# Kernel optimization log

Measured on AMD Instinct MI355X. Metric: run time of the kernel, lower is better.

## Reference

```python
import jax, jax.numpy as jnp
import numpy as np

N = 100000   # num_embeddings
D = 128      # embedding_dims
E = 128      # edge_output_size
S = 2048     # number of streaming interactions
W_DECAY = 1.0  # Decayer w, decay_method='exp': f(dt) = exp(-w*dt)


def setup_inputs() -> dict:
    key = jax.random.key(0)
    ks = jax.random.split(key, 20)
    def nrm(k, shape, s):
        return jax.random.normal(k, shape, jnp.float32) * s
    sD = 1.0 / np.sqrt(D)
    sE = 1.0 / np.sqrt(E)
    return {
        'heads': jax.random.randint(ks[0], (S,), 0, N, dtype=jnp.int32),
        'tails': jax.random.randint(ks[1], (S,), 0, N, dtype=jnp.int32),
        'times': jnp.sort(jax.random.uniform(ks[2], (S,), jnp.float32) * 100.0),
        # node state tables (nn.Embedding weights in the original)
        'node_rep': nrm(ks[3], (N, D), 0.1),
        'cell_head': nrm(ks[4], (N, D), 0.1),
        'hidden_head': nrm(ks[5], (N, D), 0.1),
        'cell_tail': nrm(ks[6], (N, D), 0.1),
        'hidden_tail': nrm(ks[7], (N, D), 0.1),
        # Edge_updater_nn head / tail: act(rep_h @ W1 + rep_t @ W2 + b)
        'Weh1': nrm(ks[8], (D, E), sD), 'Weh2': nrm(ks[9], (D, E), sD), 'beh': jnp.zeros((E,), jnp.float32),
        'Wet1': nrm(ks[10], (D, E), sD), 'Wet2': nrm(ks[11], (D, E), sD), 'bet': jnp.zeros((E,), jnp.float32),
        # TLSTM head (time-decayed LSTM cell)
        'Wxh': nrm(ks[12], (E, 4 * D), sE), 'Whh': nrm(ks[13], (D, 4 * D), sD), 'bh': jnp.zeros((4 * D,), jnp.float32),
        'Wdh': nrm(ks[14], (D, D), sD), 'bdh': jnp.zeros((D,), jnp.float32),
        # TLSTM tail
        'Wxt': nrm(ks[15], (E, 4 * D), sE), 'Wht': nrm(ks[16], (D, 4 * D), sD), 'bt': jnp.zeros((4 * D,), jnp.float32),
        'Wdt': nrm(ks[17], (D, D), sD), 'bdt': jnp.zeros((D,), jnp.float32),
        # Combiner: tanh(h_head @ Wc1 + h_tail @ Wc2)
        'Wc1': nrm(ks[18], (D, D), sD), 'Wc2': nrm(ks[19], (D, D), sD),
    }


def _tlstm(x, c, h, decay, Wx, Wh, b, Wd, bd):
    # Time-aware LSTM: decompose short-term memory, decay it by elapsed time, recombine.
    cs = jnp.tanh(c @ Wd + bd)      # short-term memory component
    c_adj = c - cs + cs * decay      # adjusted previous cell
    z = x @ Wx + h @ Wh + b          # [4D] gate pre-activations
    i, f, o, g = jnp.split(z, 4)
    i = jax.nn.sigmoid(i); f = jax.nn.sigmoid(f); o = jax.nn.sigmoid(o)
    g = jnp.tanh(g)
    c_new = f * c_adj + i * g
    h_new = o * jnp.tanh(c_new)
    return c_new, h_new


def reference(heads, tails, times, node_rep, cell_head, hidden_head, cell_tail, hidden_tail,
              Weh1, Weh2, beh, Wet1, Wet2, bet,
              Wxh, Whh, bh, Wdh, bdh, Wxt, Wht, bt, Wdt, bdt, Wc1, Wc2):
    recent = jnp.zeros((node_rep.shape[0],), jnp.float32)  # recent_timestamp, init 0

    def step(state, ev):
        rep, ch, hh, ct, ht, rt = state
        h_i, t_i, tm = ev
        rep_h = rep[h_i]                    # gather current reps
        rep_t = rep[t_i]
        dec_h = jnp.exp(-W_DECAY * (tm - rt[h_i]))   # decayer(delta_t)
        dec_t = jnp.exp(-W_DECAY * (tm - rt[t_i]))
        edge_h = jnp.tanh(rep_h @ Weh1 + rep_t @ Weh2 + beh)  # edge_updater_head
        edge_t = jnp.tanh(rep_h @ Wet1 + rep_t @ Wet2 + bet)  # edge_updater_tail
        c_h, h_h = _tlstm(edge_h, ch[h_i], hh[h_i], dec_h, Wxh, Whh, bh, Wdh, bdh)
        c_t, h_t = _tlstm(edge_t, ct[t_i], ht[t_i], dec_t, Wxt, Wht, bt, Wdt, bdt)
        new_rep_h = jnp.tanh(h_h @ Wc1 + ht[h_i] @ Wc2)  # combiner(head hidden, tail hidden)
        new_rep_t = jnp.tanh(hh[t_i] @ Wc1 + h_t @ Wc2)
        # scatter updated state (head written before tail, matching original ordering)
        rep = rep.at[h_i].set(new_rep_h).at[t_i].set(new_rep_t)
        ch = ch.at[h_i].set(c_h); hh = hh.at[h_i].set(h_h)
        ct = ct.at[t_i].set(c_t); ht = ht.at[t_i].set(h_t)
        rt = rt.at[h_i].set(tm).at[t_i].set(tm)
        # if_updated=0: emit pre-update representations for this interaction
        return (rep, ch, hh, ct, ht, rt), (rep_h, rep_t)

    state0 = (node_rep, cell_head, hidden_head, cell_tail, hidden_tail, recent)
    _, (out_h, out_t) = jax.lax.scan(step, state0, (heads, tails, times))
    return jnp.stack([out_h, out_t])  # [2, S, D]
```

## Files before the change

kernel.cpp:

```cpp
#include <hip/hip_runtime.h>
#include <hip/hip_cooperative_groups.h>
#include <math.h>

namespace cg = cooperative_groups;

#define DD 128
#define G 8
#define TPB 512
#define NBLK_MAX 256
#define SMAX 2048

__device__ __forceinline__ float sigmoidf(float x) { return 1.0f / (1.0f + expf(-x)); }

__global__ __launch_bounds__(64) void pred_kernel(
    const int* __restrict__ heads, const int* __restrict__ tails, int S,
    int* __restrict__ ph, int* __restrict__ pt) {
  const int j = blockIdx.x;
  if (j >= S) return;
  const int myh = heads[j], myt = tails[j];
  const int lane = threadIdx.x;
  int mph = -1, mpt = -1;
#pragma unroll 4
  for (int i = lane; i < j; i += 64) {
    int a = heads[i], b = tails[i];
    if (a == myh || b == myh) mph = i;
    if (a == myt || b == myt) mpt = i;
  }
#pragma unroll
  for (int off = 32; off > 0; off >>= 1) {
    mph = max(mph, __shfl_down(mph, off));
    mpt = max(mpt, __shfl_down(mpt, off));
  }
  if (lane == 0) { ph[j] = mph; pt[j] = mpt; }
}

__global__ __launch_bounds__(1024) void finalize_kernel(
    int S, const int* __restrict__ phg, const int* __restrict__ ptg,
    int* __restrict__ order, int* __restrict__ level_off, int* __restrict__ n_levels) {
  __shared__ int lvl[SMAX], ph[SMAX], pt[SMAX], cnt[SMAX];
  __shared__ int changed, maxl;
  const int tid = threadIdx.x;

  for (int j = tid; j < S; j += 1024) { ph[j] = phg[j]; pt[j] = ptg[j]; lvl[j] = 1; }
  __syncthreads();

  for (int it = 0; it < S + 2; ++it) {
    if (tid == 0) changed = 0;
    __syncthreads();
    for (int j = tid; j < S; j += 1024) {
      int l = 1;
      int a = ph[j]; if (a >= 0) l = lvl[a] + 1;
      int b = pt[j]; if (b >= 0) { int lb = lvl[b] + 1; if (lb > l) l = lb; }
      if (l != lvl[j]) { lvl[j] = l; changed = 1; }
    }
    __syncthreads();
    if (!changed) break;
    __syncthreads();
  }

  if (tid == 0) maxl = 0;
  __syncthreads();
  for (int j = tid; j < S; j += 1024) atomicMax(&maxl, lvl[j]);
  __syncthreads();
  const int M = maxl;

  for (int l = tid; l < M; l += 1024) cnt[l] = 0;
  __syncthreads();
  for (int j = tid; j < S; j += 1024) atomicAdd(&cnt[lvl[j] - 1], 1);
  __syncthreads();
  if (tid == 0) {
    int run = 0;
    level_off[0] = 0;
    for (int l = 0; l < M; ++l) { run += cnt[l]; level_off[l + 1] = run; }
    n_levels[0] = M;
  }
  __syncthreads();

  for (int l = tid; l < M; l += 1024) cnt[l] = 0;
  __syncthreads();
  for (int j = tid; j < S; j += 1024) {
    int lv = lvl[j] - 1;
    int pos = level_off[lv] + atomicAdd(&cnt[lv], 1);
    order[pos] = j;
  }
}

struct PParams {
  const int* heads; const int* tails; const float* times;
  float* node_rep; float* cell_head; float* hidden_head; float* cell_tail; float* hidden_tail;
  const float* Weh1; const float* Weh2; const float* beh;
  const float* Wet1; const float* Wet2; const float* bet;
  const float* Wxh; const float* Whh; const float* bh; const float* Wdh; const float* bdh;
  const float* Wxt; const float* Wht; const float* bt; const float* Wdt; const float* bdt;
  const float* Wc1; const float* Wc2;
  float* out; float* rt;
  const int* order; const int* level_off; const int* n_levels;
  int S;
};

__global__ __launch_bounds__(TPB) void process_kernel(PParams p) {
  cg::grid_group grid = cg::this_grid();
  const int tid = threadIdx.x;
  const int d0 = (int)((blockIdx.x * 37u) & 127u);

  __shared__ __align__(16) float S_[16384];
  __shared__ int sIdx[G], hIdx[G], tIdx[G];
  __shared__ float tmv[G], decHs[G], decTs[G];

  const int O_REPH = 0,    O_REPT = 1024, O_CHS = 2048, O_CTS = 3072;
  const int O_ZH   = 0,    O_ZT   = 4096;
  const int O_HHS  = 8192, O_HTS  = 9216, O_HTH = 10240, O_HHT = 11264;
  const int O_EH   = 12288, O_ET  = 13312;
  const int O_CAH  = 14336, O_CAT = 15360;

  int nlv = p.n_levels[0];
  if (nlv < 0) nlv = 0;
  if (nlv > SMAX) nlv = SMAX;

  for (int lv = 0; lv < nlv; ++lv) {
    const int beg = p.level_off[lv], end = p.level_off[lv + 1];

    for (int base = beg + (int)blockIdx.x * G; base < end; base += (int)gridDim.x * G) {
      const int ng = min(G, end - base);
      __syncthreads();
      if (tid < ng) {
        int s = p.order[base + tid]; sIdx[tid] = s;
        int h = p.heads[s], t = p.tails[s];
        hIdx[tid] = h; tIdx[tid] = t;
        float tm = p.times[s]; tmv[tid] = tm;
        decHs[tid] = expf(-(tm - p.rt[h]));
        decTs[tid] = expf(-(tm - p.rt[t]));
      }
      __syncthreads();

      {
        const int d = tid & 127;
        for (int g = tid >> 7; g < ng; g += 4) {
          const size_t oh = (size_t)hIdx[g] * DD + d;
          const size_t ot = (size_t)tIdx[g] * DD + d;
          const int b = d * 8 + g;
          float rh = p.node_rep[oh];
          S_[O_REPH + b] = rh; p.out[(size_t)sIdx[g] * DD + d] = rh;
          S_[O_CHS + b] = p.cell_head[oh];
          S_[O_HHS + b] = p.hidden_head[oh];
          S_[O_HTH + b] = p.hidden_tail[oh];
          float rt_ = p.node_rep[ot];
          S_[O_REPT + b] = rt_; p.out[(size_t)(p.S + sIdx[g]) * DD + d] = rt_;
          S_[O_CTS + b] = p.cell_tail[ot];
          S_[O_HTS + b] = p.hidden_tail[ot];
          S_[O_HHT + b] = p.hidden_head[ot];
        }
      }
      __syncthreads();

      {
        const int role = tid >> 7, e = tid & 127;
        if (role == 0) {
          float bv = p.beh[e];
          float a[8];
#pragma unroll
          for (int g = 0; g < 8; ++g) a[g] = bv;
#pragma unroll 8
          for (int i = 0; i < DD; ++i) {
            const int d = (i + d0) & 127;
            float w1 = p.Weh1[d * DD + e], w2 = p.Weh2[d * DD + e];
            float4 rh0 = *(const float4*)&S_[O_REPH + d * 8];
            float4 rh1 = *(const float4*)&S_[O_REPH + d * 8 + 4];
            float4 rt0 = *(const float4*)&S_[O_REPT + d * 8];
            float4 rt1 = *(const float4*)&S_[O_REPT + d * 8 + 4];
            a[0] += rh0.x * w1 + rt0.x * w2; a[1] += rh0.y * w1 + rt0.y * w2;
            a[2] += rh0.z * w1 + rt0.z * w2; a[3] += rh0.w * w1 + rt0.w * w2;
            a[4] += rh1.x * w1 + rt1.x * w2; a[5] += rh1.y * w1 + rt1.y * w2;
            a[6] += rh1.z * w1 + rt1.z * w2; a[7] += rh1.w * w1 + rt1.w * w2;
          }
          float4 o0, o1;
          o0.x = tanhf(a[0]); o0.y = tanhf(a[1]); o0.z = tanhf(a[2]); o0.w = tanhf(a[3]);
          o1.x = tanhf(a[4]); o1.y = tanhf(a[5]); o1.z = tanhf(a[6]); o1.w = tanhf(a[7]);
          *(float4*)&S_[O_EH + e * 8] = o0;
          *(float4*)&S_[O_EH + e * 8 + 4] = o1;
        } else if (role == 1) {
          float bv = p.bet[e];
          float a[8];
#pragma unroll
          for (int g = 0; g < 8; ++g) a[g] = bv;
#pragma unroll 8
          for (int i = 0; i < DD; ++i) {
            const int d = (i + d0) & 127;
            float w1 = p.Wet1[d * DD + e], w2 = p.Wet2[d * DD + e];
            float4 rh0 = *(const float4*)&S_[O_REPH + d * 8];
            float4 rh1 = *(const float4*)&S_[O_REPH + d * 8 + 4];
            float4 rt0 = *(const float4*)&S_[O_REPT + d * 8];
            float4 rt1 = *(const float4*)&S_[O_REPT + d * 8 + 4];
            a[0] += rh0.x * w1 + rt0.x * w2; a[1] += rh0.y * w1 + rt0.y * w2;
            a[2] += rh0.z * w1 + rt0.z * w2; a[3] += rh0.w * w1 + rt0.w * w2;
            a[4] += rh1.x * w1 + rt1.x * w2; a[5] += rh1.y * w1 + rt1.y * w2;
            a[6] += rh1.z * w1 + rt1.z * w2; a[7] += rh1.w * w1 + rt1.w * w2;
          }
          float4 o0, o1;
          o0.x = tanhf(a[0]); o0.y = tanhf(a[1]); o0.z = tanhf(a[2]); o0.w = tanhf(a[3]);
          o1.x = tanhf(a[4]); o1.y = tanhf(a[5]); o1.z = tanhf(a[6]); o1.w = tanhf(a[7]);
          *(float4*)&S_[O_ET + e * 8] = o0;
          *(float4*)&S_[O_ET + e * 8 + 4] = o1;
        } else if (role == 2) {
          float bv = p.bdh[e];
          float a[8];
#pragma unroll
          for (int g = 0; g < 8; ++g) a[g] = bv;
#pragma unroll 8
          for (int i = 0; i < DD; ++i) {
            const int d = (i + d0) & 127;
            float wd = p.Wdh[d * DD + e];
            float4 c0 = *(const float4*)&S_[O_CHS + d * 8];
            float4 c1 = *(const float4*)&S_[O_CHS + d * 8 + 4];
            a[0] += c0.x * wd; a[1] += c0.y * wd; a[2] += c0.z * wd; a[3] += c0.w * wd;
            a[4] += c1.x * wd; a[5] += c1.y * wd; a[6] += c1.z * wd; a[7] += c1.w * wd;
          }
          float o[8];
#pragma unroll
          for (int g = 0; g < 8; ++g) {
            float cs = tanhf(a[g]);
            o[g] = S_[O_CHS + e * 8 + g] - cs + cs * decHs[g];
          }
          *(float4*)&S_[O_CAH + e * 8]     = make_float4(o[0], o[1], o[2], o[3]);
          *(float4*)&S_[O_CAH + e * 8 + 4] = make_float4(o[4], o[5], o[6], o[7]);
        } else {
          float bv = p.bdt[e];
          float a[8];
#pragma unroll
          for (int g = 0; g < 8; ++g) a[g] = bv;
#pragma unroll 8
          for (int i = 0; i < DD; ++i) {
            const int d = (i + d0) & 127;
            float wd = p.Wdt[d * DD + e];
            float4 c0 = *(const float4*)&S_[O_CTS + d * 8];
            float4 c1 = *(const float4*)&S_[O_CTS + d * 8 + 4];
            a[0] += c0.x * wd; a[1] += c0.y * wd; a[2] += c0.z * wd; a[3] += c0.w * wd;
            a[4] += c1.x * wd; a[5] += c1.y * wd; a[6] += c1.z * wd; a[7] += c1.w * wd;
          }
          float o[8];
#pragma unroll
          for (int g = 0; g < 8; ++g) {
            float cs = tanhf(a[g]);
            o[g] = S_[O_CTS + e * 8 + g] - cs + cs * decTs[g];
          }
          *(float4*)&S_[O_CAT + e * 8]     = make_float4(o[0], o[1], o[2], o[3]);
          *(float4*)&S_[O_CAT + e * 8 + 4] = make_float4(o[4], o[5], o[6], o[7]);
        }
      }
      __syncthreads();

      {
        const int c = tid;
        float bhv = p.bh[c], btv = p.bt[c];
        float h[8], t8[8];
#pragma unroll
        for (int g = 0; g < 8; ++g) { h[g] = bhv; t8[g] = btv; }
#pragma unroll 4
        for (int i = 0; i < DD; ++i) {
          const int d = (i + d0) & 127;
          float wxh = p.Wxh[d * 512 + c], whh = p.Whh[d * 512 + c];
          float wxt = p.Wxt[d * 512 + c], wht = p.Wht[d * 512 + c];
          float4 ex0 = *(const float4*)&S_[O_EH + d * 8];
          float4 ex1 = *(const float4*)&S_[O_EH + d * 8 + 4];
          float4 hx0 = *(const float4*)&S_[O_HHS + d * 8];
          float4 hx1 = *(const float4*)&S_[O_HHS + d * 8 + 4];
          float4 et0 = *(const float4*)&S_[O_ET + d * 8];
          float4 et1 = *(const float4*)&S_[O_ET + d * 8 + 4];
          float4 ht0 = *(const float4*)&S_[O_HTS + d * 8];
          float4 ht1 = *(const float4*)&S_[O_HTS + d * 8 + 4];
          h[0] += ex0.x * wxh + hx0.x * whh; h[1] += ex0.y * wxh + hx0.y * whh;
          h[2] += ex0.z * wxh + hx0.z * whh; h[3] += ex0.w * wxh + hx0.w * whh;
          h[4] += ex1.x * wxh + hx1.x * whh; h[5] += ex1.y * wxh + hx1.y * whh;
          h[6] += ex1.z * wxh + hx1.z * whh; h[7] += ex1.w * wxh + hx1.w * whh;
          t8[0] += et0.x * wxt + ht0.x * wht; t8[1] += et0.y * wxt + ht0.y * wht;
          t8[2] += et0.z * wxt + ht0.z * wht; t8[3] += et0.w * wxt + ht0.w * wht;
          t8[4] += et1.x * wxt + ht1.x * wht; t8[5] += et1.y * wxt + ht1.y * wht;
          t8[6] += et1.z * wxt + ht1.z * wht; t8[7] += et1.w * wxt + ht1.w * wht;
        }
        *(float4*)&S_[O_ZH + c * 8]     = make_float4(h[0], h[1], h[2], h[3]);
        *(float4*)&S_[O_ZH + c * 8 + 4] = make_float4(h[4], h[5], h[6], h[7]);
        *(float4*)&S_[O_ZT + c * 8]     = make_float4(t8[0], t8[1], t8[2], t8[3]);
        *(float4*)&S_[O_ZT + c * 8 + 4] = make_float4(t8[4], t8[5], t8[6], t8[7]);
      }
      __syncthreads();

      {
        const int side = tid >> 8, sub = (tid >> 7) & 1, e = tid & 127;
        const int zo = side ? O_ZT : O_ZH;
        const int co = side ? O_CAT : O_CAH;
        const int no = side ? O_ET : O_EH;
        float* ctab = side ? p.cell_tail : p.cell_head;
        float* htab = side ? p.hidden_tail : p.hidden_head;
        for (int q = 0; q < 4; ++q) {
          int g = sub + 2 * q;
          if (g >= ng) continue;
          float iv = sigmoidf(S_[zo + e * 8 + g]);
          float fv = sigmoidf(S_[zo + (128 + e) * 8 + g]);
          float ov = sigmoidf(S_[zo + (256 + e) * 8 + g]);
          float gv = tanhf(S_[zo + (384 + e) * 8 + g]);
          float cadj = S_[co + e * 8 + g];
          float cn = fv * cadj + iv * gv;
          float hn = ov * tanhf(cn);
          S_[no + e * 8 + g] = hn;
          int node = side ? tIdx[g] : hIdx[g];
          ctab[(size_t)node * DD + e] = cn;
          htab[(size_t)node * DD + e] = hn;
        }
        if (tid < 2 * G) {
          int g = tid & (G - 1);
          if (g < ng) p.rt[(tid >= G) ? tIdx[g] : hIdx[g]] = tmv[g];
        }
      }
      __syncthreads();

      {
        const int role = tid >> 7, e = tid & 127;
        if (role == 0) {
          float a[8];
#pragma unroll
          for (int g = 0; g < 8; ++g) a[g] = 0.f;
#pragma unroll 8
          for (int i = 0; i < DD; ++i) {
            const int d = (i + d0) & 127;
            float w1 = p.Wc1[d * DD + e], w2 = p.Wc2[d * DD + e];
            float4 x0 = *(const float4*)&S_[O_EH + d * 8];
            float4 x1 = *(const float4*)&S_[O_EH + d * 8 + 4];
            float4 y0 = *(const float4*)&S_[O_HTH + d * 8];
            float4 y1 = *(const float4*)&S_[O_HTH + d * 8 + 4];
            a[0] += x0.x * w1 + y0.x * w2; a[1] += x0.y * w1 + y0.y * w2;
            a[2] += x0.z * w1 + y0.z * w2; a[3] += x0.w * w1 + y0.w * w2;
            a[4] += x1.x * w1 + y1.x * w2; a[5] += x1.y * w1 + y1.y * w2;
            a[6] += x1.z * w1 + y1.z * w2; a[7] += x1.w * w1 + y1.w * w2;
          }
#pragma unroll
          for (int g = 0; g < 8; ++g)
            if (g < ng && hIdx[g] != tIdx[g])
              p.node_rep[(size_t)hIdx[g] * DD + e] = tanhf(a[g]);
        } else if (role == 1) {
          float a[8];
#pragma unroll
          for (int g = 0; g < 8; ++g) a[g] = 0.f;
#pragma unroll 8
          for (int i = 0; i < DD; ++i) {
            const int d = (i + d0) & 127;
            float w1 = p.Wc1[d * DD + e], w2 = p.Wc2[d * DD + e];
            float4 x0 = *(const float4*)&S_[O_HHT + d * 8];
            float4 x1 = *(const float4*)&S_[O_HHT + d * 8 + 4];
            float4 y0 = *(const float4*)&S_[O_ET + d * 8];
            float4 y1 = *(const float4*)&S_[O_ET + d * 8 + 4];
            a[0] += x0.x * w1 + y0.x * w2; a[1] += x0.y * w1 + y0.y * w2;
            a[2] += x0.z * w1 + y0.z * w2; a[3] += x0.w * w1 + y0.w * w2;
            a[4] += x1.x * w1 + y1.x * w2; a[5] += x1.y * w1 + y1.y * w2;
            a[6] += x1.z * w1 + y1.z * w2; a[7] += x1.w * w1 + y1.w * w2;
          }
#pragma unroll
          for (int g = 0; g < 8; ++g)
            if (g < ng)
              p.node_rep[(size_t)tIdx[g] * DD + e] = tanhf(a[g]);
        }
      }
    }
    __threadfence();
    grid.sync();
  }
}

extern "C" void kernel_launch(void* const* d_in, const int* in_sizes, int n_in,
                              void* d_out, int out_size, void* d_ws, size_t ws_size,
                              hipStream_t stream) {
  const int* heads = (const int*)d_in[0];
  const int* tails = (const int*)d_in[1];
  const float* times = (const float*)d_in[2];
  float* node_rep    = (float*)d_in[3];
  float* cell_head   = (float*)d_in[4];
  float* hidden_head = (float*)d_in[5];
  float* cell_tail   = (float*)d_in[6];
  float* hidden_tail = (float*)d_in[7];
  const float* Weh1 = (const float*)d_in[8];
  const float* Weh2 = (const float*)d_in[9];
  const float* beh  = (const float*)d_in[10];
  const float* Wet1 = (const float*)d_in[11];
  const float* Wet2 = (const float*)d_in[12];
  const float* bet  = (const float*)d_in[13];
  const float* Wxh  = (const float*)d_in[14];
  const float* Whh  = (const float*)d_in[15];
  const float* bh   = (const float*)d_in[16];
  const float* Wdh  = (const float*)d_in[17];
  const float* bdh  = (const float*)d_in[18];
  const float* Wxt  = (const float*)d_in[19];
  const float* Wht  = (const float*)d_in[20];
  const float* bt   = (const float*)d_in[21];
  const float* Wdt  = (const float*)d_in[22];
  const float* bdt  = (const float*)d_in[23];
  const float* Wc1  = (const float*)d_in[24];
  const float* Wc2  = (const float*)d_in[25];

  const int S = in_sizes[0];
  const int N = in_sizes[3] / DD;

  char* ws = (char*)d_ws;
  float* rt = (float*)ws;
  size_t rtBytes = (((size_t)N * 4) + 511) & ~(size_t)511;
  int* order     = (int*)(ws + rtBytes);
  int* level_off = order + SMAX;
  int* n_levels  = level_off + SMAX + 1;
  int* ph        = n_levels + 64;
  int* pt        = ph + SMAX;

  hipMemsetAsync(rt, 0, (size_t)N * 4, stream);
  pred_kernel<<<S, 64, 0, stream>>>(heads, tails, S, ph, pt);
  finalize_kernel<<<1, 1024, 0, stream>>>(S, ph, pt, order, level_off, n_levels);

  PParams p;
  p.heads = heads; p.tails = tails; p.times = times;
  p.node_rep = node_rep; p.cell_head = cell_head; p.hidden_head = hidden_head;
  p.cell_tail = cell_tail; p.hidden_tail = hidden_tail;
  p.Weh1 = Weh1; p.Weh2 = Weh2; p.beh = beh;
  p.Wet1 = Wet1; p.Wet2 = Wet2; p.bet = bet;
  p.Wxh = Wxh; p.Whh = Whh; p.bh = bh; p.Wdh = Wdh; p.bdh = bdh;
  p.Wxt = Wxt; p.Wht = Wht; p.bt = bt; p.Wdt = Wdt; p.bdt = bdt;
  p.Wc1 = Wc1; p.Wc2 = Wc2;
  p.out = (float*)d_out; p.rt = rt;
  p.order = order; p.level_off = level_off; p.n_levels = n_levels;
  p.S = S;

  void* args[] = { (void*)&p };

  int dev = 0; hipGetDevice(&dev);
  int nCU = 0;
  hipDeviceGetAttribute(&nCU, hipDeviceAttributeMultiprocessorCount, dev);
  if (nCU <= 0) nCU = 256;
  int maxBlkPerCU = 0;
  hipOccupancyMaxActiveBlocksPerMultiprocessor(&maxBlkPerCU, process_kernel, TPB, 0);
  if (maxBlkPerCU < 1) maxBlkPerCU = 1;
  long long cap = (long long)nCU * (long long)maxBlkPerCU;
  int grid = (int)(cap < NBLK_MAX ? cap : NBLK_MAX);
  if (grid < 1) grid = nCU;

  hipError_t err = hipLaunchCooperativeKernel(process_kernel, dim3(grid), dim3(TPB),
                                              args, 0, stream);
  if (err != hipSuccess && grid > 128) {
    err = hipLaunchCooperativeKernel(process_kernel, dim3(128), dim3(TPB), args, 0, stream);
  }
  if (err != hipSuccess && grid > 64) {
    err = hipLaunchCooperativeKernel(process_kernel, dim3(64), dim3(TPB), args, 0, stream);
  }
}
```

Before: 714.1 us.

## Split each dependency level into three grid-synced phases with batched row tiles

The per-level work is restructured into three grid-wide phases: edge/decay/gather jobs over 64-row tiles, LSTM gate jobs over 16-row tiles per side, and combiner jobs. This replaces the old scheme where each block processed groups of 8 interactions end to end. Weights are first transposed into a k4-interleaved float4 layout in workspace, and intermediates are staged in global buffers. The grid cap rises to 512 blocks with launch bounds of one block per CU. The aim is to spread each level's work across more blocks and batch more rows per weight load, at the cost of two extra grid syncs per level and extra global-memory traffic for the intermediates.

Measured after the change: 1.432 ms. +100.5%, slower.

```diff
diff --git a/kernel.cpp b/kernel.cpp
--- a/kernel.cpp
+++ b/kernel.cpp
@@ -5,10 +5,9 @@
 namespace cg = cooperative_groups;
 
 #define DD 128
-#define G 8
 #define TPB 512
-#define NBLK_MAX 256
 #define SMAX 2048
+#define NBLK_MAX 512
 
 __device__ __forceinline__ float sigmoidf(float x) { return 1.0f / (1.0f + expf(-x)); }
 
@@ -88,30 +87,51 @@
 struct PParams {
   const int* heads; const int* tails; const float* times;
   float* node_rep; float* cell_head; float* hidden_head; float* cell_tail; float* hidden_tail;
-  const float* Weh1; const float* Weh2; const float* beh;
-  const float* Wet1; const float* Wet2; const float* bet;
-  const float* Wxh; const float* Whh; const float* bh; const float* Wdh; const float* bdh;
-  const float* Wxt; const float* Wht; const float* bt; const float* Wdt; const float* bdt;
-  const float* Wc1; const float* Wc2;
+  const float* beh; const float* bet; const float* bh; const float* bt;
+  const float* bdh; const float* bdt;
+  const float* Wsrc[12];
+  float* Wt[12];
+  float* EH; float* ET; float* CADJH; float* CADJT;
+  float* HTHold; float* HHTold; float* HNH; float* HNT;
   float* out; float* rt;
   const int* order; const int* level_off; const int* n_levels;
   int S;
 };
 
-__global__ __launch_bounds__(TPB) void process_kernel(PParams p) {
+#define FMA4(j, a, w) \
+  acc[j] += (a).x * (w).x + (a).y * (w).y + (a).z * (w).z + (a).w * (w).w
+
+__global__ __launch_bounds__(TPB, 1) void process_kernel(PParams p) {
   cg::grid_group grid = cg::this_grid();
   const int tid = threadIdx.x;
-  const int d0 = (int)((blockIdx.x * 37u) & 127u);
-
-  __shared__ __align__(16) float S_[16384];
-  __shared__ int sIdx[G], hIdx[G], tIdx[G];
-  __shared__ float tmv[G], decHs[G], decTs[G];
-
-  const int O_REPH = 0,    O_REPT = 1024, O_CHS = 2048, O_CTS = 3072;
-  const int O_ZH   = 0,    O_ZT   = 4096;
-  const int O_HHS  = 8192, O_HTS  = 9216, O_HTH = 10240, O_HHT = 11264;
-  const int O_EH   = 12288, O_ET  = 13312;
-  const int O_CAH  = 14336, O_CAT = 15360;
+  const int bid = (int)blockIdx.x;
+  const int nb  = (int)gridDim.x;
+
+  __shared__ float Z[16 * 512];
+  __shared__ int hL[64], tL[64], sL[64];
+  __shared__ float decL[64];
+
+  {
+    const long total = 8L * 4096 + 4L * 16384;
+    for (long i = (long)bid * TPB + tid; i < total; i += (long)nb * TPB) {
+      int mat, k4, e, E;
+      if (i < 32768) {
+        mat = (int)(i >> 12); int rem = (int)i & 4095; k4 = rem >> 7; e = rem & 127; E = 128;
+      } else {
+        long i2 = i - 32768; mat = 8 + (int)(i2 >> 14); int rem = (int)i2 & 16383;
+        k4 = rem >> 9; e = rem & 511; E = 512;
+      }
+      const float* Wm = p.Wsrc[mat];
+      float4 v;
+      v.x = Wm[(4 * k4 + 0) * E + e];
+      v.y = Wm[(4 * k4 + 1) * E + e];
+      v.z = Wm[(4 * k4 + 2) * E + e];
+      v.w = Wm[(4 * k4 + 3) * E + e];
+      *(float4*)&p.Wt[mat][((long)(k4 * E + e)) * 4] = v;
+    }
+  }
+  __threadfence();
+  grid.sync();
 
   int nlv = p.n_levels[0];
   if (nlv < 0) nlv = 0;
@@ -119,244 +139,249 @@
 
   for (int lv = 0; lv < nlv; ++lv) {
     const int beg = p.level_off[lv], end = p.level_off[lv + 1];
-
-    for (int base = beg + (int)blockIdx.x * G; base < end; base += (int)gridDim.x * G) {
-      const int ng = min(G, end - base);
-      __syncthreads();
-      if (tid < ng) {
-        int s = p.order[base + tid]; sIdx[tid] = s;
-        int h = p.heads[s], t = p.tails[s];
-        hIdx[tid] = h; tIdx[tid] = t;
-        float tm = p.times[s]; tmv[tid] = tm;
-        decHs[tid] = expf(-(tm - p.rt[h]));
-        decTs[tid] = expf(-(tm - p.rt[t]));
-      }
-      __syncthreads();
-
-      {
-        const int d = tid & 127;
-        for (int g = tid >> 7; g < ng; g += 4) {
-          const size_t oh = (size_t)hIdx[g] * DD + d;
-          const size_t ot = (size_t)tIdx[g] * DD + d;
-          const int b = d * 8 + g;
-          float rh = p.node_rep[oh];
-          S_[O_REPH + b] = rh; p.out[(size_t)sIdx[g] * DD + d] = rh;
-          S_[O_CHS + b] = p.cell_head[oh];
-          S_[O_HHS + b] = p.hidden_head[oh];
-          S_[O_HTH + b] = p.hidden_tail[oh];
-          float rt_ = p.node_rep[ot];
-          S_[O_REPT + b] = rt_; p.out[(size_t)(p.S + sIdx[g]) * DD + d] = rt_;
-          S_[O_CTS + b] = p.cell_tail[ot];
-          S_[O_HTS + b] = p.hidden_tail[ot];
-          S_[O_HHT + b] = p.hidden_head[ot];
-        }
-      }
-      __syncthreads();
-
-      {
-        const int role = tid >> 7, e = tid & 127;
-        if (role == 0) {
-          float bv = p.beh[e];
-          float a[8];
-#pragma unroll
-          for (int g = 0; g < 8; ++g) a[g] = bv;
-#pragma unroll 8
-          for (int i = 0; i < DD; ++i) {
-            const int d = (i + d0) & 127;
-            float w1 = p.Weh1[d * DD + e], w2 = p.Weh2[d * DD + e];
-            float4 rh0 = *(const float4*)&S_[O_REPH + d * 8];
-            float4 rh1 = *(const float4*)&S_[O_REPH + d * 8 + 4];
-            float4 rt0 = *(const float4*)&S_[O_REPT + d * 8];
-            float4 rt1 = *(const float4*)&S_[O_REPT + d * 8 + 4];
-            a[0] += rh0.x * w1 + rt0.x * w2; a[1] += rh0.y * w1 + rt0.y * w2;
-            a[2] += rh0.z * w1 + rt0.z * w2; a[3] += rh0.w * w1 + rt0.w * w2;
-            a[4] += rh1.x * w1 + rt1.x * w2; a[5] += rh1.y * w1 + rt1.y * w2;
-            a[6] += rh1.z * w1 + rt1.z * w2; a[7] += rh1.w * w1 + rt1.w * w2;
+    const int M = end - beg;
+    const int nmt64 = (M + 63) >> 6;
+    const int nmt16 = (M + 15) >> 4;
+
+    for (int job = bid; job < 5 * nmt64; job += nb) {
+      const int type = job / nmt64;
+      const int mt = job - type * nmt64;
+      const int r0 = mt << 6;
+      __syncthreads();
+      if (tid < 64) {
+        int r = r0 + tid;
+        int s = -1, h = 0, t = 0;
+        float dec = 1.0f;
+        if (r < M) {
+          s = p.order[beg + r]; h = p.heads[s]; t = p.tails[s];
+          if (type == 2) dec = expf(-(p.times[s] - p.rt[h]));
+          else if (type == 3) dec = expf(-(p.times[s] - p.rt[t]));
+        }
+        sL[tid] = s; hL[tid] = h; tL[tid] = t; decL[tid] = dec;
+      }
+      __syncthreads();
+
+      const int e = tid & 127;
+      const int rg = tid >> 7;
+
+      if (type <= 1) {
+        const float* W1 = p.Wt[type ? 2 : 0];
+        const float* W2 = p.Wt[type ? 3 : 1];
+        const float* bias = type ? p.bet : p.beh;
+        float acc[16];
+        float bv = bias[e];
+#pragma unroll
+        for (int j = 0; j < 16; ++j) acc[j] = bv;
+        unsigned offs[16];
+#pragma unroll
+        for (int j = 0; j < 16; ++j)
+          offs[j] = (unsigned)__builtin_amdgcn_readfirstlane(hL[rg * 16 + j]) * 128u;
+#pragma unroll 2
+        for (int k4 = 0; k4 < 32; ++k4) {
+          float4 w = *(const float4*)&W1[(k4 * 128 + e) * 4];
+#pragma unroll
+          for (int j = 0; j < 16; ++j) {
+            float4 a = *(const float4*)&p.node_rep[(size_t)offs[j] + (k4 << 2)];
+            FMA4(j, a, w);
           }
-          float4 o0, o1;
-          o0.x = tanhf(a[0]); o0.y = tanhf(a[1]); o0.z = tanhf(a[2]); o0.w = tanhf(a[3]);
-          o1.x = tanhf(a[4]); o1.y = tanhf(a[5]); o1.z = tanhf(a[6]); o1.w = tanhf(a[7]);
-          *(float4*)&S_[O_EH + e * 8] = o0;
-          *(float4*)&S_[O_EH + e * 8 + 4] = o1;
-        } else if (role == 1) {
-          float bv = p.bet[e];
-          float a[8];
-#pragma unroll
-          for (int g = 0; g < 8; ++g) a[g] = bv;
-#pragma unroll 8
-          for (int i = 0; i < DD; ++i) {
-            const int d = (i + d0) & 127;
-            float w1 = p.Wet1[d * DD + e], w2 = p.Wet2[d * DD + e];
-            float4 rh0 = *(const float4*)&S_[O_REPH + d * 8];
-            float4 rh1 = *(const float4*)&S_[O_REPH + d * 8 + 4];
-            float4 rt0 = *(const float4*)&S_[O_REPT + d * 8];
-            float4 rt1 = *(const float4*)&S_[O_REPT + d * 8 + 4];
-            a[0] += rh0.x * w1 + rt0.x * w2; a[1] += rh0.y * w1 + rt0.y * w2;
-            a[2] += rh0.z * w1 + rt0.z * w2; a[3] += rh0.w * w1 + rt0.w * w2;
-            a[4] += rh1.x * w1 + rt1.x * w2; a[5] += rh1.y * w1 + rt1.y * w2;
-            a[6] += rh1.z * w1 + rt1.z * w2; a[7] += rh1.w * w1 + rt1.w * w2;
+        }
+#pragma unroll
+        for (int j = 0; j < 16; ++j)
+          offs[j] = (unsigned)__builtin_amdgcn_readfirstlane(tL[rg * 16 + j]) * 128u;
+#pragma unroll 2
+        for (int k4 = 0; k4 < 32; ++k4) {
+          float4 w = *(const float4*)&W2[(k4 * 128 + e) * 4];
+#pragma unroll
+          for (int j = 0; j < 16; ++j) {
+            float4 a = *(const float4*)&p.node_rep[(size_t)offs[j] + (k4 << 2)];
+            FMA4(j, a, w);
           }
-          float4 o0, o1;
-          o0.x = tanhf(a[0]); o0.y = tanhf(a[1]); o0.z = tanhf(a[2]); o0.w = tanhf(a[3]);
-          o1.x = tanhf(a[4]); o1.y = tanhf(a[5]); o1.z = tanhf(a[6]); o1.w = tanhf(a[7]);
-          *(float4*)&S_[O_ET + e * 8] = o0;
-          *(float4*)&S_[O_ET + e * 8 + 4] = o1;
-        } else if (role == 2) {
-          float bv = p.bdh[e];
-          float a[8];
-#pragma unroll
-          for (int g = 0; g < 8; ++g) a[g] = bv;
-#pragma unroll 8
-          for (int i = 0; i < DD; ++i) {
-            const int d = (i + d0) & 127;
-            float wd = p.Wdh[d * DD + e];
-            float4 c0 = *(const float4*)&S_[O_CHS + d * 8];
-            float4 c1 = *(const float4*)&S_[O_CHS + d * 8 + 4];
-            a[0] += c0.x * wd; a[1] += c0.y * wd; a[2] += c0.z * wd; a[3] += c0.w * wd;
-            a[4] += c1.x * wd; a[5] += c1.y * wd; a[6] += c1.z * wd; a[7] += c1.w * wd;
+        }
+        float* dst = type ? p.ET : p.EH;
+#pragma unroll
+        for (int j = 0; j < 16; ++j) {
+          int r = r0 + rg * 16 + j;
+          if (r < M) dst[(size_t)r * 128 + e] = tanhf(acc[j]);
+        }
+      } else if (type <= 3) {
+        const float* W = p.Wt[type == 2 ? 4 : 5];
+        const float* bias = (type == 2) ? p.bdh : p.bdt;
+        const float* ctab = (type == 2) ? p.cell_head : p.cell_tail;
+        const int* nodeL = (type == 2) ? hL : tL;
+        float acc[16];
+        float bv = bias[e];
+#pragma unroll
+        for (int j = 0; j < 16; ++j) acc[j] = bv;
+        unsigned offs[16];
+#pragma unroll
+        for (int j = 0; j < 16; ++j)
+          offs[j] = (unsigned)__builtin_amdgcn_readfirstlane(nodeL[rg * 16 + j]) * 128u;
+#pragma unroll 2
+        for (int k4 = 0; k4 < 32; ++k4) {
+          float4 w = *(const float4*)&W[(k4 * 128 + e) * 4];
+#pragma unroll
+          for (int j = 0; j < 16; ++j) {
+            float4 a = *(const float4*)&ctab[(size_t)offs[j] + (k4 << 2)];
+            FMA4(j, a, w);
           }
-          float o[8];
-#pragma unroll
-          for (int g = 0; g < 8; ++g) {
-            float cs = tanhf(a[g]);
-            o[g] = S_[O_CHS + e * 8 + g] - cs + cs * decHs[g];
+        }
+        float* dst = (type == 2) ? p.CADJH : p.CADJT;
+#pragma unroll
+        for (int j = 0; j < 16; ++j) {
+          int lr = rg * 16 + j, r = r0 + lr;
+          if (r < M) {
+            float cs = tanhf(acc[j]);
+            float c = ctab[(size_t)offs[j] + e];
+            dst[(size_t)r * 128 + e] = c - cs + cs * decL[lr];
           }
-          *(float4*)&S_[O_CAH + e * 8]     = make_float4(o[0], o[1], o[2], o[3]);
-          *(float4*)&S_[O_CAH + e * 8 + 4] = make_float4(o[4], o[5], o[6], o[7]);
-        } else {
-          float bv = p.bdt[e];
-          float a[8];
-#pragma unroll
-          for (int g = 0; g < 8; ++g) a[g] = bv;
-#pragma unroll 8
-          for (int i = 0; i < DD; ++i) {
-            const int d = (i + d0) & 127;
-            float wd = p.Wdt[d * DD + e];
-            float4 c0 = *(const float4*)&S_[O_CTS + d * 8];
-            float4 c1 = *(const float4*)&S_[O_CTS + d * 8 + 4];
-            a[0] += c0.x * wd; a[1] += c0.y * wd; a[2] += c0.z * wd; a[3] += c0.w * wd;
-            a[4] += c1.x * wd; a[5] += c1.y * wd; a[6] += c1.z * wd; a[7] += c1.w * wd;
-          }
-          float o[8];
-#pragma unroll
-          for (int g = 0; g < 8; ++g) {
-            float cs = tanhf(a[g]);
-            o[g] = S_[O_CTS + e * 8 + g] - cs + cs * decTs[g];
-          }
-          *(float4*)&S_[O_CAT + e * 8]     = make_float4(o[0], o[1], o[2], o[3]);
-          *(float4*)&S_[O_CAT + e * 8 + 4] = make_float4(o[4], o[5], o[6], o[7]);
-        }
-      }
-      __syncthreads();
-
-      {
-        const int c = tid;
-        float bhv = p.bh[c], btv = p.bt[c];
-        float h[8], t8[8];
-#pragma unroll
-        for (int g = 0; g < 8; ++g) { h[g] = bhv; t8[g] = btv; }
+        }
+      } else {
 #pragma unroll 4
-        for (int i = 0; i < DD; ++i) {
-          const int d = (i + d0) & 127;
-          float wxh = p.Wxh[d * 512 + c], whh = p.Whh[d * 512 + c];
-          float wxt = p.Wxt[d * 512 + c], wht = p.Wht[d * 512 + c];
-          float4 ex0 = *(const float4*)&S_[O_EH + d * 8];
-          float4 ex1 = *(const float4*)&S_[O_EH + d * 8 + 4];
-          float4 hx0 = *(const float4*)&S_[O_HHS + d * 8];
-          float4 hx1 = *(const float4*)&S_[O_HHS + d * 8 + 4];
-          float4 et0 = *(const float4*)&S_[O_ET + d * 8];
-          float4 et1 = *(const float4*)&S_[O_ET + d * 8 + 4];
-          float4 ht0 = *(const float4*)&S_[O_HTS + d * 8];
-          float4 ht1 = *(const float4*)&S_[O_HTS + d * 8 + 4];
-          h[0] += ex0.x * wxh + hx0.x * whh; h[1] += ex0.y * wxh + hx0.y * whh;
-          h[2] += ex0.z * wxh + hx0.z * whh; h[3] += ex0.w * wxh + hx0.w * whh;
-          h[4] += ex1.x * wxh + hx1.x * whh; h[5] += ex1.y * wxh + hx1.y * whh;
-          h[6] += ex1.z * wxh + hx1.z * whh; h[7] += ex1.w * wxh + hx1.w * whh;
-          t8[0] += et0.x * wxt + ht0.x * wht; t8[1] += et0.y * wxt + ht0.y * wht;
-          t8[2] += et0.z * wxt + ht0.z * wht; t8[3] += et0.w * wxt + ht0.w * wht;
-          t8[4] += et1.x * wxt + ht1.x * wht; t8[5] += et1.y * wxt + ht1.y * wht;
-          t8[6] += et1.z * wxt + ht1.z * wht; t8[7] += et1.w * wxt + ht1.w * wht;
-        }
-        *(float4*)&S_[O_ZH + c * 8]     = make_float4(h[0], h[1], h[2], h[3]);
-        *(float4*)&S_[O_ZH + c * 8 + 4] = make_float4(h[4], h[5], h[6], h[7]);
-        *(float4*)&S_[O_ZT + c * 8]     = make_float4(t8[0], t8[1], t8[2], t8[3]);
-        *(float4*)&S_[O_ZT + c * 8 + 4] = make_float4(t8[4], t8[5], t8[6], t8[7]);
-      }
-      __syncthreads();
-
-      {
-        const int side = tid >> 8, sub = (tid >> 7) & 1, e = tid & 127;
-        const int zo = side ? O_ZT : O_ZH;
-        const int co = side ? O_CAT : O_CAH;
-        const int no = side ? O_ET : O_EH;
-        float* ctab = side ? p.cell_tail : p.cell_head;
-        float* htab = side ? p.hidden_tail : p.hidden_head;
-        for (int q = 0; q < 4; ++q) {
-          int g = sub + 2 * q;
-          if (g >= ng) continue;
-          float iv = sigmoidf(S_[zo + e * 8 + g]);
-          float fv = sigmoidf(S_[zo + (128 + e) * 8 + g]);
-          float ov = sigmoidf(S_[zo + (256 + e) * 8 + g]);
-          float gv = tanhf(S_[zo + (384 + e) * 8 + g]);
-          float cadj = S_[co + e * 8 + g];
+        for (int j = 0; j < 16; ++j) {
+          int lr = rg * 16 + j, r = r0 + lr;
+          if (r >= M) continue;
+          int s = sL[lr];
+          unsigned ho = (unsigned)hL[lr] * 128u, to = (unsigned)tL[lr] * 128u;
+          p.out[(size_t)s * 128 + e] = p.node_rep[(size_t)ho + e];
+          p.out[(size_t)(p.S + s) * 128 + e] = p.node_rep[(size_t)to + e];
+          p.HTHold[(size_t)r * 128 + e] = p.hidden_tail[(size_t)ho + e];
+          p.HHTold[(size_t)r * 128 + e] = p.hidden_head[(size_t)to + e];
+        }
+      }
+    }
+    __threadfence();
+    grid.sync();
+
+    for (int job = bid; job < 2 * nmt16; job += nb) {
+      const int side = job & 1;
+      const int mt = job >> 1;
+      const int r0 = mt << 4;
+      __syncthreads();
+      if (tid < 16) {
+        int r = r0 + tid;
+        int s = -1, h = 0, t = 0;
+        if (r < M) { s = p.order[beg + r]; h = p.heads[s]; t = p.tails[s]; }
+        sL[tid] = s; hL[tid] = h; tL[tid] = t;
+      }
+      __syncthreads();
+
+      const int c = tid;
+      const float* TX = p.Wt[side ? 10 : 8];
+      const float* TH = p.Wt[side ? 11 : 9];
+      const float* bias = side ? p.bt : p.bh;
+      const float* X = side ? p.ET : p.EH;
+      float* ctab = side ? p.cell_tail : p.cell_head;
+      float* htab = side ? p.hidden_tail : p.hidden_head;
+      const int* nodeL = side ? tL : hL;
+
+      float acc[16];
+      float bv = bias[c];
+#pragma unroll
+      for (int j = 0; j < 16; ++j) acc[j] = bv;
+
+#pragma unroll 2
+      for (int k4 = 0; k4 < 32; ++k4) {
+        float4 w = *(const float4*)&TX[((long)(k4 * 512 + c)) * 4];
+#pragma unroll
+        for (int j = 0; j < 16; ++j) {
+          float4 a = *(const float4*)&X[(size_t)(r0 + j) * 128 + (k4 << 2)];
+          FMA4(j, a, w);
+        }
+      }
+      unsigned offs[16];
+#pragma unroll
+      for (int j = 0; j < 16; ++j)
+        offs[j] = (unsigned)__builtin_amdgcn_readfirstlane(nodeL[j]) * 128u;
+#pragma unroll 2
+      for (int k4 = 0; k4 < 32; ++k4) {
+        float4 w = *(const float4*)&TH[((long)(k4 * 512 + c)) * 4];
+#pragma unroll
+        for (int j = 0; j < 16; ++j) {
+          float4 a = *(const float4*)&htab[(size_t)offs[j] + (k4 << 2)];
+          FMA4(j, a, w);
+        }
+      }
+#pragma unroll
+      for (int j = 0; j < 16; ++j) Z[j * 512 + c] = acc[j];
+      __syncthreads();
+
+      const float* cadjB = side ? p.CADJT : p.CADJH;
+      float* hnB = side ? p.HNT : p.HNH;
+#pragma unroll
+      for (int q = 0; q < 4; ++q) {
+        int idx = q * 512 + tid;
+        int lr = idx >> 7, e2 = idx & 127;
+        int r = r0 + lr;
+        if (r < M) {
+          float iv = sigmoidf(Z[lr * 512 + e2]);
+          float fv = sigmoidf(Z[lr * 512 + 128 + e2]);
+          float ov = sigmoidf(Z[lr * 512 + 256 + e2]);
+          float gv = tanhf(Z[lr * 512 + 384 + e2]);
+          float cadj = cadjB[(size_t)r * 128 + e2];
           float cn = fv * cadj + iv * gv;
           float hn = ov * tanhf(cn);
-          S_[no + e * 8 + g] = hn;
-          int node = side ? tIdx[g] : hIdx[g];
-          ctab[(size_t)node * DD + e] = cn;
-          htab[(size_t)node * DD + e] = hn;
-        }
-        if (tid < 2 * G) {
-          int g = tid & (G - 1);
-          if (g < ng) p.rt[(tid >= G) ? tIdx[g] : hIdx[g]] = tmv[g];
-        }
-      }
-      __syncthreads();
-
-      {
-        const int role = tid >> 7, e = tid & 127;
-        if (role == 0) {
-          float a[8];
-#pragma unroll
-          for (int g = 0; g < 8; ++g) a[g] = 0.f;
-#pragma unroll 8
-          for (int i = 0; i < DD; ++i) {
-            const int d = (i + d0) & 127;
-            float w1 = p.Wc1[d * DD + e], w2 = p.Wc2[d * DD + e];
-            float4 x0 = *(const float4*)&S_[O_EH + d * 8];
-            float4 x1 = *(const float4*)&S_[O_EH + d * 8 + 4];
-            float4 y0 = *(const float4*)&S_[O_HTH + d * 8];
-            float4 y1 = *(const float4*)&S_[O_HTH + d * 8 + 4];
-            a[0] += x0.x * w1 + y0.x * w2; a[1] += x0.y * w1 + y0.y * w2;
-            a[2] += x0.z * w1 + y0.z * w2; a[3] += x0.w * w1 + y0.w * w2;
-            a[4] += x1.x * w1 + y1.x * w2; a[5] += x1.y * w1 + y1.y * w2;
-            a[6] += x1.z * w1 + y1.z * w2; a[7] += x1.w * w1 + y1.w * w2;
-          }
-#pragma unroll
-          for (int g = 0; g < 8; ++g)
-            if (g < ng && hIdx[g] != tIdx[g])
-              p.node_rep[(size_t)hIdx[g] * DD + e] = tanhf(a[g]);
-        } else if (role == 1) {
-          float a[8];
-#pragma unroll
-          for (int g = 0; g < 8; ++g) a[g] = 0.f;
-#pragma unroll 8
-          for (int i = 0; i < DD; ++i) {
-            const int d = (i + d0) & 127;
-            float w1 = p.Wc1[d * DD + e], w2 = p.Wc2[d * DD + e];
-            float4 x0 = *(const float4*)&S_[O_HHT + d * 8];
-            float4 x1 = *(const float4*)&S_[O_HHT + d * 8 + 4];
-            float4 y0 = *(const float4*)&S_[O_ET + d * 8];
-            float4 y1 = *(const float4*)&S_[O_ET + d * 8 + 4];
-            a[0] += x0.x * w1 + y0.x * w2; a[1] += x0.y * w1 + y0.y * w2;
-            a[2] += x0.z * w1 + y0.z * w2; a[3] += x0.w * w1 + y0.w * w2;
-            a[4] += x1.x * w1 + y1.x * w2; a[5] += x1.y * w1 + y1.y * w2;
-            a[6] += x1.z * w1 + y1.z * w2; a[7] += x1.w * w1 + y1.w * w2;
-          }
-#pragma unroll
-          for (int g = 0; g < 8; ++g)
-            if (g < ng)
-              p.node_rep[(size_t)tIdx[g] * DD + e] = tanhf(a[g]);
+          unsigned no = (unsigned)nodeL[lr] * 128u;
+          ctab[(size_t)no + e2] = cn;
+          htab[(size_t)no + e2] = hn;
+          hnB[(size_t)r * 128 + e2] = hn;
+        }
+      }
+      if (tid < 16) {
+        int r = r0 + tid;
+        if (r < M) p.rt[nodeL[tid]] = p.times[sL[tid]];
+      }
+    }
+    __threadfence();
+    grid.sync();
+
+    for (int job = bid; job < 2 * nmt64; job += nb) {
+      const int side = job & 1;
+      const int mt = job >> 1;
+      const int r0 = mt << 6;
+      __syncthreads();
+      if (tid < 64) {
+        int r = r0 + tid;
+        int s = -1, h = 0, t = 0;
+        if (r < M) { s = p.order[beg + r]; h = p.heads[s]; t = p.tails[s]; }
+        sL[tid] = s; hL[tid] = h; tL[tid] = t;
+      }
+      __syncthreads();
+
+      const int e = tid & 127;
+      const int rg = tid >> 7;
+      const float* A1 = side ? p.HHTold : p.HNH;
+      const float* A2 = side ? p.HNT : p.HTHold;
+      const float* W1 = p.Wt[6];
+      const float* W2 = p.Wt[7];
+      float acc[16];
+#pragma unroll
+      for (int j = 0; j < 16; ++j) acc[j] = 0.0f;
+
+#pragma unroll 2
+      for (int k4 = 0; k4 < 32; ++k4) {
+        float4 w = *(const float4*)&W1[(k4 * 128 + e) * 4];
+#pragma unroll
+        for (int j = 0; j < 16; ++j) {
+          float4 a = *(const float4*)&A1[(size_t)(r0 + rg * 16 + j) * 128 + (k4 << 2)];
+          FMA4(j, a, w);
+        }
+      }
+#pragma unroll 2
+      for (int k4 = 0; k4 < 32; ++k4) {
+        float4 w = *(const float4*)&W2[(k4 * 128 + e) * 4];
+#pragma unroll
+        for (int j = 0; j < 16; ++j) {
+          float4 a = *(const float4*)&A2[(size_t)(r0 + rg * 16 + j) * 128 + (k4 << 2)];
+          FMA4(j, a, w);
+        }
+      }
+#pragma unroll
+      for (int j = 0; j < 16; ++j) {
+        int lr = rg * 16 + j, r = r0 + lr;
+        if (r < M) {
+          int h = hL[lr], t = tL[lr];
+          if (side) p.node_rep[(size_t)t * 128 + e] = tanhf(acc[j]);
+          else if (h != t) p.node_rep[(size_t)h * 128 + e] = tanhf(acc[j]);
         }
       }
     }
@@ -376,53 +401,61 @@
   float* hidden_head = (float*)d_in[5];
   float* cell_tail   = (float*)d_in[6];
   float* hidden_tail = (float*)d_in[7];
-  const float* Weh1 = (const float*)d_in[8];
-  const float* Weh2 = (const float*)d_in[9];
-  const float* beh  = (const float*)d_in[10];
-  const float* Wet1 = (const float*)d_in[11];
-  const float* Wet2 = (const float*)d_in[12];
-  const float* bet  = (const float*)d_in[13];
-  const float* Wxh  = (const float*)d_in[14];
-  const float* Whh  = (const float*)d_in[15];
-  const float* bh   = (const float*)d_in[16];
-  const float* Wdh  = (const float*)d_in[17];
-  const float* bdh  = (const float*)d_in[18];
-  const float* Wxt  = (const float*)d_in[19];
-  const float* Wht  = (const float*)d_in[20];
-  const float* bt   = (const float*)d_in[21];
-  const float* Wdt  = (const float*)d_in[22];
-  const float* bdt  = (const float*)d_in[23];
-  const float* Wc1  = (const float*)d_in[24];
-  const float* Wc2  = (const float*)d_in[25];
 
   const int S = in_sizes[0];
   const int N = in_sizes[3] / DD;
 
   char* ws = (char*)d_ws;
+  size_t off = 0;
   float* rt = (float*)ws;
-  size_t rtBytes = (((size_t)N * 4) + 511) & ~(size_t)511;
-  int* order     = (int*)(ws + rtBytes);
-  int* level_off = order + SMAX;
-  int* n_levels  = level_off + SMAX + 1;
-  int* ph        = n_levels + 64;
-  int* pt        = ph + SMAX;
-
-  hipMemsetAsync(rt, 0, (size_t)N * 4, stream);
-  pred_kernel<<<S, 64, 0, stream>>>(heads, tails, S, ph, pt);
-  finalize_kernel<<<1, 1024, 0, stream>>>(S, ph, pt, order, level_off, n_levels);
+  off = (((size_t)N * 4) + 511) & ~(size_t)511;
+  int* order     = (int*)(ws + off); off += (size_t)SMAX * 4;
+  int* level_off = (int*)(ws + off); off += (size_t)(SMAX + 1) * 4;
+  int* n_levels  = (int*)(ws + off); off += 64 * 4;
+  int* ph        = (int*)(ws + off); off += (size_t)SMAX * 4;
+  int* pt        = (int*)(ws + off); off += (size_t)SMAX * 4;
+  off = (off + 255) & ~(size_t)255;
 
   PParams p;
   p.heads = heads; p.tails = tails; p.times = times;
   p.node_rep = node_rep; p.cell_head = cell_head; p.hidden_head = hidden_head;
   p.cell_tail = cell_tail; p.hidden_tail = hidden_tail;
-  p.Weh1 = Weh1; p.Weh2 = Weh2; p.beh = beh;
-  p.Wet1 = Wet1; p.Wet2 = Wet2; p.bet = bet;
-  p.Wxh = Wxh; p.Whh = Whh; p.bh = bh; p.Wdh = Wdh; p.bdh = bdh;
-  p.Wxt = Wxt; p.Wht = Wht; p.bt = bt; p.Wdt = Wdt; p.bdt = bdt;
-  p.Wc1 = Wc1; p.Wc2 = Wc2;
+  p.beh = (const float*)d_in[10]; p.bet = (const float*)d_in[13];
+  p.bh  = (const float*)d_in[16]; p.bt  = (const float*)d_in[21];
+  p.bdh = (const float*)d_in[18]; p.bdt = (const float*)d_in[23];
+  p.Wsrc[0] = (const float*)d_in[8];
+  p.Wsrc[1] = (const float*)d_in[9];
+  p.Wsrc[2] = (const float*)d_in[11];
+  p.Wsrc[3] = (const float*)d_in[12];
+  p.Wsrc[4] = (const float*)d_in[17];
+  p.Wsrc[5] = (const float*)d_in[22];
+  p.Wsrc[6] = (const float*)d_in[24];
+  p.Wsrc[7] = (const float*)d_in[25];
+  p.Wsrc[8] = (const float*)d_in[14];
+  p.Wsrc[9] = (const float*)d_in[15];
+  p.Wsrc[10] = (const float*)d_in[19];
+  p.Wsrc[11] = (const float*)d_in[20];
+
+  for (int m = 0; m < 12; ++m) {
+    size_t n = (m < 8) ? 16384 : 65536;
+    p.Wt[m] = (float*)(ws + off); off += n * 4;
+  }
+  p.EH     = (float*)(ws + off); off += (size_t)SMAX * 128 * 4;
+  p.ET     = (float*)(ws + off); off += (size_t)SMAX * 128 * 4;
+  p.CADJH  = (float*)(ws + off); off += (size_t)SMAX * 128 * 4;
+  p.CADJT  = (float*)(ws + off); off += (size_t)SMAX * 128 * 4;
+  p.HTHold = (float*)(ws + off); off += (size_t)SMAX * 128 * 4;
+  p.HHTold = (float*)(ws + off); off += (size_t)SMAX * 128 * 4;
+  p.HNH    = (float*)(ws + off); off += (size_t)SMAX * 128 * 4;
+  p.HNT    = (float*)(ws + off); off += (size_t)SMAX * 128 * 4;
+
   p.out = (float*)d_out; p.rt = rt;
   p.order = order; p.level_off = level_off; p.n_levels = n_levels;
   p.S = S;
+
+  hipMemsetAsync(rt, 0, (size_t)N * 4, stream);
+  pred_kernel<<<S, 64, 0, stream>>>(heads, tails, S, ph, pt);
+  finalize_kernel<<<1, 1024, 0, stream>>>(S, ph, pt, order, level_off, n_levels);
 
   void* args[] = { (void*)&p };
 
@@ -439,10 +472,10 @@
 
   hipError_t err = hipLaunchCooperativeKernel(process_kernel, dim3(grid), dim3(TPB),
                                               args, 0, stream);
+  if (err != hipSuccess && grid > 256) {
+    err = hipLaunchCooperativeKernel(process_kernel, dim3(256), dim3(TPB), args, 0, stream);
+  }
   if (err != hipSuccess && grid > 128) {
     err = hipLaunchCooperativeKernel(process_kernel, dim3(128), dim3(TPB), args, 0, stream);
   }
-  if (err != hipSuccess && grid > 64) {
-    err = hipLaunchCooperativeKernel(process_kernel, dim3(64), dim3(TPB), args, 0, stream);
-  }
 }
```
